# Optimization experiments

Hardware: AMD Instinct MI355X
Metric: run time of the kernel (lower is better)

## Reference

```python
import jax, jax.numpy as jnp
import numpy as np

K = 2  # top-k experts per token


def setup_inputs() -> dict:
    key = jax.random.key(0)
    k1, k2, k3, k4 = jax.random.split(key, 4)
    B, S, D, E = 4, 4096, 1024, 64
    x = jax.random.normal(k1, (B, S, D), dtype=jnp.float32)
    gate_w = jax.random.normal(k2, (E, D), dtype=jnp.float32) * (1.0 / np.sqrt(D))
    noise_weight = jax.random.normal(k3, (E,), dtype=jnp.float32) * 0.02
    noise = jax.random.normal(k4, (B, S, E), dtype=jnp.float32)  # randn_like(logits) * noisy_std(=1.0)
    return {"x": x, "gate_w": gate_w, "noise_weight": noise_weight, "noise": noise}


def reference(x, gate_w, noise_weight, noise):
    E = gate_w.shape[0]
    # logits = x @ W^T  -> [B, S, E]
    logits = jnp.einsum("bsd,ed->bse", x, gate_w)
    logits_noisy = logits + noise * noise_weight  # noisy_std = 1.0 folded into `noise`
    top_vals, top_idx = jax.lax.top_k(logits_noisy, K)  # [B,S,K]
    # scatter top-k logits into a -inf mask, then softmax over experts
    keep = jax.nn.one_hot(top_idx, E, dtype=jnp.bool_).any(axis=-2)  # [B,S,E]
    neg_inf = jnp.finfo(logits_noisy.dtype).min
    sparse = jnp.where(keep, logits_noisy, neg_inf)
    weights = jax.nn.softmax(sparse, axis=-1)
    return weights, top_idx
```

## Files before the change

kernel.cpp:

```cpp
#include <hip/hip_runtime.h>
#include <math.h>


#define DDIM 1024
#define NEXP 64
#define NTOK 16384
#define TILE_T 256
#define BK 32
#define XROW 384

__global__ __launch_bounds__(256, 2)
void gemm_partial_kernel(const float* __restrict__ x,
                         const float* __restrict__ gate_w,
                         float* __restrict__ part,
                         int nsplit, int ksize)
{
    __shared__ float xT[BK * XROW];

    const int tid   = threadIdx.x;
    const int tile  = blockIdx.x & 63;
    const int split = blockIdx.x >> 6;
    const int tokBase = tile * TILE_T;
    const int k0 = split * ksize;

    const int tc = tid & 31;
    const int te = tid >> 5;

    float acc[8][8];
    #pragma unroll
    for (int i = 0; i < 8; ++i)
        #pragma unroll
        for (int r = 0; r < 8; ++r) acc[i][r] = 0.f;

    const int s_tok = tid >> 3;
    const int s_u   = tid & 7;

    for (int kc = 0; kc < ksize; kc += BK) {
        const int kg = k0 + kc;
        __syncthreads();
        #pragma unroll
        for (int p = 0; p < 8; ++p) {
            const int tok = p * 32 + s_tok;
            const float4 v = *(const float4*)&x[(size_t)(tokBase + tok) * DDIM + kg + s_u * 4];
            const int gbase = (tok >> 3) * 12 + (tok & 7);
            xT[(s_u * 4 + 0) * XROW + gbase] = v.x;
            xT[(s_u * 4 + 1) * XROW + gbase] = v.y;
            xT[(s_u * 4 + 2) * XROW + gbase] = v.z;
            xT[(s_u * 4 + 3) * XROW + gbase] = v.w;
        }
        __syncthreads();

        #pragma unroll 2
        for (int kk = 0; kk < BK / 4; ++kk) {
            float4 wf[8];
            #pragma unroll
            for (int r = 0; r < 8; ++r)
                wf[r] = *(const float4*)&gate_w[(size_t)(te * 8 + r) * DDIM + kg + kk * 4];
            #pragma unroll
            for (int j = 0; j < 4; ++j) {
                const float4 xa = *(const float4*)&xT[(kk * 4 + j) * XROW + tc * 12];
                const float4 xb = *(const float4*)&xT[(kk * 4 + j) * XROW + tc * 12 + 4];
                const float xv[8] = {xa.x, xa.y, xa.z, xa.w, xb.x, xb.y, xb.z, xb.w};
                #pragma unroll
                for (int r = 0; r < 8; ++r) {
                    const float wv = ((const float*)&wf[r])[j];
                    #pragma unroll
                    for (int i = 0; i < 8; ++i)
                        acc[i][r] = fmaf(xv[i], wv, acc[i][r]);
                }
            }
        }
    }

    #pragma unroll
    for (int i = 0; i < 8; ++i) {
        float* dst = &part[((size_t)split * NTOK + tokBase + tc * 8 + i) * NEXP + te * 8];
        float4 a = {acc[i][0], acc[i][1], acc[i][2], acc[i][3]};
        float4 b = {acc[i][4], acc[i][5], acc[i][6], acc[i][7]};
        *(float4*)dst = a;
        *(float4*)(dst + 4) = b;
    }
}

__global__ __launch_bounds__(256)
void reduce_topk_kernel(const float* __restrict__ part,
                        const float* __restrict__ noise_weight,
                        const float* __restrict__ noise,
                        float* __restrict__ out_w,
                        float* __restrict__ out_i,
                        int nsplit)
{
    const int lane = threadIdx.x & 63;
    const int wv   = threadIdx.x >> 6;
    const int token = blockIdx.x * 4 + wv;

    float sum = 0.f;
    for (int s = 0; s < nsplit; ++s)
        sum += part[((size_t)s * NTOK + token) * NEXP + lane];

    const float ln = fmaf(noise[(size_t)token * NEXP + lane], noise_weight[lane], sum);

    float v1 = ln; int i1 = lane;
    #pragma unroll
    for (int off = 32; off > 0; off >>= 1) {
        const float vo = __shfl_xor(v1, off, 64);
        const int   io = __shfl_xor(i1, off, 64);
        if (vo > v1 || (vo == v1 && io < i1)) { v1 = vo; i1 = io; }
    }
    float v2 = (lane == i1) ? -3.4e38f : ln; int i2 = lane;
    #pragma unroll
    for (int off = 32; off > 0; off >>= 1) {
        const float vo = __shfl_xor(v2, off, 64);
        const int   io = __shfl_xor(i2, off, 64);
        if (vo > v2 || (vo == v2 && io < i2)) { v2 = vo; i2 = io; }
    }

    const float d   = expf(v2 - v1);
    const float inv = 1.f / (1.f + d);
    const float wgt = (lane == i1) ? inv : ((lane == i2) ? d * inv : 0.f);
    out_w[(size_t)token * NEXP + lane] = wgt;
    if (lane == 0) {
        out_i[(size_t)token * 2]     = (float)i1;
        out_i[(size_t)token * 2 + 1] = (float)i2;
    }
}

extern "C" void kernel_launch(void* const* d_in, const int* in_sizes, int n_in,
                              void* d_out, int out_size, void* d_ws, size_t ws_size,
                              hipStream_t stream) {
    const float* x     = (const float*)d_in[0];
    const float* gw    = (const float*)d_in[1];
    const float* nwt   = (const float*)d_in[2];
    const float* noise = (const float*)d_in[3];
    float* out_w = (float*)d_out;
    float* out_i = (float*)d_out + (size_t)NTOK * NEXP;
    float* part  = (float*)d_ws;

    int S = 8;
    while (S > 1 && (size_t)S * NTOK * NEXP * 4 > ws_size) S >>= 1;
    const int ksize = DDIM / S;

    hipLaunchKernelGGL(gemm_partial_kernel, dim3(64 * S), dim3(256), 0, stream,
                       x, gw, part, S, ksize);
    hipLaunchKernelGGL(reduce_topk_kernel, dim3(NTOK / 4), dim3(256), 0, stream,
                       part, nwt, noise, out_w, out_i, S);
}
```

Before: 144.3 us.

## Replace FP32 FMA gating GEMM with split-bf16 MFMA using a pre-split weight image

The scalar FP32 FMA gating GEMM is replaced by bf16 MFMA instructions. Both operands are split into three bf16 parts (hi/mid/lo) and six cross-product MFMAs are summed to approximate FP32 accuracy. A small prep kernel writes the gate weights in an MFMA-friendly split layout, and this image is streamed into LDS with global_load_lds. x rows are double-buffered in registers, the K-split is fixed at 4, and the partial outputs are still reduced in the top-k kernel. The aim is to move the matmul onto the matrix cores. The cost is an extra launch, more MFMA work per element, and a small risk that top-k selection changes on near-ties because of the reduced precision.

```diff
diff --git a/kernel.cpp b/kernel.cpp
--- a/kernel.cpp
+++ b/kernel.cpp
@@ -5,97 +5,151 @@
 #define DDIM 1024
 #define NEXP 64
 #define NTOK 16384
-#define TILE_T 256
-#define BK 32
-#define XROW 384
-
-__global__ __launch_bounds__(256, 2)
-void gemm_partial_kernel(const float* __restrict__ x,
-                         const float* __restrict__ gate_w,
-                         float* __restrict__ part,
-                         int nsplit, int ksize)
+#define NSPLIT 4
+#define CPB 4
+
+typedef float f4 __attribute__((ext_vector_type(4)));
+typedef short s8 __attribute__((ext_vector_type(8)));
+typedef unsigned int u32;
+
+static __device__ __forceinline__ void split3(float f, short& h, short& m, short& l) {
+    const u32 uf = __float_as_uint(f);
+    h = (short)(uf >> 16);
+    const float r1 = f - __uint_as_float(uf & 0xffff0000u);
+    const u32 u1 = __float_as_uint(r1);
+    m = (short)(u1 >> 16);
+    const float r2 = r1 - __uint_as_float(u1 & 0xffff0000u);
+    l = (short)(__float_as_uint(r2) >> 16);
+}
+
+static __device__ __forceinline__ void gl_lds16(const void* g, void* l) {
+    __builtin_amdgcn_global_load_lds(
+        (const __attribute__((address_space(1))) u32*)g,
+        (__attribute__((address_space(3))) u32*)l, 16, 0, 0);
+}
+
+__global__ __launch_bounds__(256)
+void w_prep(const float* __restrict__ gw, short* __restrict__ wimg) {
+    const int uid = blockIdx.x * 256 + threadIdx.x;
+    const int c   = uid >> 9;
+    const int kk  = (uid >> 8) & 1;
+    const int e   = (uid >> 2) & 63;
+    const int q   = uid & 3;
+    const int k0  = c * 64 + kk * 32 + q * 8;
+    const float* src = gw + (size_t)e * DDIM + k0;
+    s8 hv, mv, lv;
+    #pragma unroll
+    for (int j = 0; j < 8; ++j) {
+        short h, m, l;
+        split3(src[j], h, m, l);
+        hv[j] = h; mv[j] = m; lv[j] = l;
+    }
+    const size_t base = (size_t)c * 1536 + (kk * 3) * 256
+                      + (e >> 4) * 64 + q * 16 + (e & 15);
+    *(s8*)(wimg + (base      ) * 8) = hv;
+    *(s8*)(wimg + (base + 256) * 8) = mv;
+    *(s8*)(wimg + (base + 512) * 8) = lv;
+}
+
+__global__ __launch_bounds__(256, 4)
+void gemm_partial(const float* __restrict__ x,
+                  const short* __restrict__ wimg,
+                  float* __restrict__ part)
 {
-    __shared__ float xT[BK * XROW];
+    __shared__ short bs[1536 * 8];
 
     const int tid   = threadIdx.x;
-    const int tile  = blockIdx.x & 63;
-    const int split = blockIdx.x >> 6;
-    const int tokBase = tile * TILE_T;
-    const int k0 = split * ksize;
-
-    const int tc = tid & 31;
-    const int te = tid >> 5;
-
-    float acc[8][8];
-    #pragma unroll
-    for (int i = 0; i < 8; ++i)
-        #pragma unroll
-        for (int r = 0; r < 8; ++r) acc[i][r] = 0.f;
-
-    const int s_tok = tid >> 3;
-    const int s_u   = tid & 7;
-
-    for (int kc = 0; kc < ksize; kc += BK) {
-        const int kg = k0 + kc;
+    const int lane  = tid & 63;
+    const int wv    = tid >> 6;
+    const int m     = lane & 15;
+    const int q     = lane >> 4;
+    const int tile  = blockIdx.x & 255;
+    const int split = blockIdx.x >> 8;
+    const int tokBase = tile * 64 + wv * 16;
+
+    const float* xrow = x + (size_t)(tokBase + m) * DDIM
+                      + split * (CPB * 64) + q * 8;
+
+    f4 acc0[4], acc1[4];
+    #pragma unroll
+    for (int t = 0; t < 4; ++t) { acc0[t] = (f4)0.f; acc1[t] = (f4)0.f; }
+
+    f4 stage[2][4];
+    stage[0][0] = *(const f4*)(xrow);
+    stage[0][1] = *(const f4*)(xrow + 4);
+    stage[0][2] = *(const f4*)(xrow + 32);
+    stage[0][3] = *(const f4*)(xrow + 36);
+
+    #pragma unroll
+    for (int cc = 0; cc < CPB; ++cc) {
+        const short* chunk = wimg + (size_t)(split * CPB + cc) * (1536 * 8);
         __syncthreads();
         #pragma unroll
-        for (int p = 0; p < 8; ++p) {
-            const int tok = p * 32 + s_tok;
-            const float4 v = *(const float4*)&x[(size_t)(tokBase + tok) * DDIM + kg + s_u * 4];
-            const int gbase = (tok >> 3) * 12 + (tok & 7);
-            xT[(s_u * 4 + 0) * XROW + gbase] = v.x;
-            xT[(s_u * 4 + 1) * XROW + gbase] = v.y;
-            xT[(s_u * 4 + 2) * XROW + gbase] = v.z;
-            xT[(s_u * 4 + 3) * XROW + gbase] = v.w;
+        for (int i = 0; i < 6; ++i) {
+            const int off = (wv * 6 + i) * 512;
+            gl_lds16(chunk + off + lane * 8, &bs[off]);
         }
         __syncthreads();
 
-        #pragma unroll 2
-        for (int kk = 0; kk < BK / 4; ++kk) {
-            float4 wf[8];
+        if (cc + 1 < CPB) {
+            const float* s = xrow + (cc + 1) * 64;
+            stage[(cc + 1) & 1][0] = *(const f4*)(s);
+            stage[(cc + 1) & 1][1] = *(const f4*)(s + 4);
+            stage[(cc + 1) & 1][2] = *(const f4*)(s + 32);
+            stage[(cc + 1) & 1][3] = *(const f4*)(s + 36);
+        }
+
+        s8 ah[2], am[2], al[2];
+        const float* sv = (const float*)stage[cc & 1];
+        #pragma unroll
+        for (int kk = 0; kk < 2; ++kk)
             #pragma unroll
-            for (int r = 0; r < 8; ++r)
-                wf[r] = *(const float4*)&gate_w[(size_t)(te * 8 + r) * DDIM + kg + kk * 4];
+            for (int j = 0; j < 8; ++j) {
+                short h, mm, l;
+                split3(sv[kk * 8 + j], h, mm, l);
+                ah[kk][j] = h; am[kk][j] = mm; al[kk][j] = l;
+            }
+
+        #pragma unroll
+        for (int kk = 0; kk < 2; ++kk) {
             #pragma unroll
-            for (int j = 0; j < 4; ++j) {
-                const float4 xa = *(const float4*)&xT[(kk * 4 + j) * XROW + tc * 12];
-                const float4 xb = *(const float4*)&xT[(kk * 4 + j) * XROW + tc * 12 + 4];
-                const float xv[8] = {xa.x, xa.y, xa.z, xa.w, xb.x, xb.y, xb.z, xb.w};
-                #pragma unroll
-                for (int r = 0; r < 8; ++r) {
-                    const float wv = ((const float*)&wf[r])[j];
-                    #pragma unroll
-                    for (int i = 0; i < 8; ++i)
-                        acc[i][r] = fmaf(xv[i], wv, acc[i][r]);
-                }
+            for (int t = 0; t < 4; ++t) {
+                const int pb = (kk * 3) * 256 + t * 64 + lane;
+                const s8 bh = *(const s8*)&bs[(pb      ) * 8];
+                const s8 bm = *(const s8*)&bs[(pb + 256) * 8];
+                const s8 bl = *(const s8*)&bs[(pb + 512) * 8];
+                acc0[t] = __builtin_amdgcn_mfma_f32_16x16x32_bf16(ah[kk], bh, acc0[t], 0, 0, 0);
+                acc1[t] = __builtin_amdgcn_mfma_f32_16x16x32_bf16(ah[kk], bm, acc1[t], 0, 0, 0);
+                acc1[t] = __builtin_amdgcn_mfma_f32_16x16x32_bf16(am[kk], bh, acc1[t], 0, 0, 0);
+                acc1[t] = __builtin_amdgcn_mfma_f32_16x16x32_bf16(ah[kk], bl, acc1[t], 0, 0, 0);
+                acc1[t] = __builtin_amdgcn_mfma_f32_16x16x32_bf16(am[kk], bm, acc1[t], 0, 0, 0);
+                acc1[t] = __builtin_amdgcn_mfma_f32_16x16x32_bf16(al[kk], bh, acc1[t], 0, 0, 0);
             }
         }
     }
 
     #pragma unroll
-    for (int i = 0; i < 8; ++i) {
-        float* dst = &part[((size_t)split * NTOK + tokBase + tc * 8 + i) * NEXP + te * 8];
-        float4 a = {acc[i][0], acc[i][1], acc[i][2], acc[i][3]};
-        float4 b = {acc[i][4], acc[i][5], acc[i][6], acc[i][7]};
-        *(float4*)dst = a;
-        *(float4*)(dst + 4) = b;
-    }
+    for (int t = 0; t < 4; ++t)
+        #pragma unroll
+        for (int r = 0; r < 4; ++r)
+            part[((size_t)split * NTOK + tokBase + q * 4 + r) * NEXP + m + 16 * t]
+                = acc0[t][r] + acc1[t][r];
 }
 
 __global__ __launch_bounds__(256)
-void reduce_topk_kernel(const float* __restrict__ part,
-                        const float* __restrict__ noise_weight,
-                        const float* __restrict__ noise,
-                        float* __restrict__ out_w,
-                        float* __restrict__ out_i,
-                        int nsplit)
+void reduce_topk(const float* __restrict__ part,
+                 const float* __restrict__ noise_weight,
+                 const float* __restrict__ noise,
+                 float* __restrict__ out_w,
+                 float* __restrict__ out_i)
 {
-    const int lane = threadIdx.x & 63;
-    const int wv   = threadIdx.x >> 6;
+    const int lane  = threadIdx.x & 63;
+    const int wv    = threadIdx.x >> 6;
     const int token = blockIdx.x * 4 + wv;
 
     float sum = 0.f;
-    for (int s = 0; s < nsplit; ++s)
+    #pragma unroll
+    for (int s = 0; s < NSPLIT; ++s)
         sum += part[((size_t)s * NTOK + token) * NEXP + lane];
 
     const float ln = fmaf(noise[(size_t)token * NEXP + lane], noise_weight[lane], sum);
@@ -134,14 +188,13 @@
     const float* noise = (const float*)d_in[3];
     float* out_w = (float*)d_out;
     float* out_i = (float*)d_out + (size_t)NTOK * NEXP;
-    float* part  = (float*)d_ws;
-
-    int S = 8;
-    while (S > 1 && (size_t)S * NTOK * NEXP * 4 > ws_size) S >>= 1;
-    const int ksize = DDIM / S;
-
-    hipLaunchKernelGGL(gemm_partial_kernel, dim3(64 * S), dim3(256), 0, stream,
-                       x, gw, part, S, ksize);
-    hipLaunchKernelGGL(reduce_topk_kernel, dim3(NTOK / 4), dim3(256), 0, stream,
-                       part, nwt, noise, out_w, out_i, S);
-}
+
+    short* wimg = (short*)d_ws;
+    float* part = (float*)((char*)d_ws + 512 * 1024);
+
+    hipLaunchKernelGGL(w_prep, dim3(32), dim3(256), 0, stream, gw, wimg);
+    hipLaunchKernelGGL(gemm_partial, dim3(256 * NSPLIT), dim3(256), 0, stream,
+                       x, wimg, part);
+    hipLaunchKernelGGL(reduce_topk, dim3(NTOK / 4), dim3(256), 0, stream,
+                       part, nwt, noise, out_w, out_i);
+}
```

Result: faster. 123.0 us (-14.8%).
